# Kernel optimization log

Measured on AMD Instinct MI355X. Metric: run time of the kernel, lower is better.

The kernel has to match this reference:

```python
import jax, jax.numpy as jnp
import numpy as np

B, LQ, LK, SIZE, H = 8, 1024, 1024, 512, 8


def setup_inputs() -> dict:
    key = jax.random.key(0)
    ks = jax.random.split(key, 12)
    scale = 1.0 / np.sqrt(SIZE)
    x = jax.random.normal(ks[0], (B, LQ, SIZE), dtype=jnp.float32)
    states = jax.random.normal(ks[1], (B, LK, SIZE), dtype=jnp.float32)
    mask = jax.random.randint(ks[2], (B, LQ, LK), 0, 2, dtype=jnp.int32)
    # Per-head full-size projections, stacked over heads: [H, size, size]
    Wq = jax.random.normal(ks[3], (H, SIZE, SIZE), dtype=jnp.float32) * scale
    bq = jnp.zeros((H, SIZE), dtype=jnp.float32)
    Wk = jax.random.normal(ks[4], (H, SIZE, SIZE), dtype=jnp.float32) * scale
    bk = jnp.zeros((H, SIZE), dtype=jnp.float32)
    Wv = jax.random.normal(ks[5], (H, SIZE, SIZE), dtype=jnp.float32) * scale
    bv = jnp.zeros((H, SIZE), dtype=jnp.float32)
    # Output projection: Linear(size*H, size); torch weight shape [size, size*H]
    Wp = jax.random.normal(ks[6], (SIZE, SIZE * H), dtype=jnp.float32) * (1.0 / np.sqrt(SIZE * H))
    bp = jnp.zeros((SIZE,), dtype=jnp.float32)
    return {"x": x, "states": states, "mask": mask,
            "Wq": Wq, "bq": bq, "Wk": Wk, "bk": bk, "Wv": Wv, "bv": bv,
            "Wp": Wp, "bp": bp}


def reference(x, states, mask, Wq, bq, Wk, bk, Wv, bv, Wp, bp):
    # torch Linear: y = x @ W.T + b ; W is [out,in] so contract over last axis 'e'
    q = jnp.einsum('bqe,hde->bhqd', x, Wq) + bq[:, None, :]       # [B,H,Lq,D]
    k = jnp.einsum('bke,hde->bhkd', states, Wk) + bk[:, None, :]  # [B,H,Lk,D]
    v = jnp.einsum('bke,hde->bhkd', states, Wv) + bv[:, None, :]  # [B,H,Lk,D]
    scores = jnp.einsum('bhqd,bhkd->bhqk', q, k) / jnp.sqrt(jnp.float32(SIZE))
    scores = jnp.where(mask[:, None, :, :] == 0, jnp.float32(-jnp.inf), scores)
    attn = jax.nn.softmax(scores, axis=-1)                        # softmax over Lk
    ctx = jnp.einsum('bhqk,bhkd->bhqd', attn, v)                  # [B,H,Lq,D]
    # concat heads in order -> [B, Lq, H*D]
    ctx = ctx.transpose(0, 2, 1, 3).reshape(B, LQ, H * SIZE)
    return ctx @ Wp.T + bp
```

## Files before the change

### kernel.cpp

```cpp
#include <hip/hip_runtime.h>
#include <hip/hip_bf16.h>

typedef __bf16 bf16_t;
typedef __bf16 bf16x8 __attribute__((ext_vector_type(8)));
typedef float f32x4 __attribute__((ext_vector_type(4)));

#define B_DIM 8
#define LQ 1024
#define LK 1024
#define DD 512
#define NH 8
#define LB 2
#define NCH 4

static __device__ __forceinline__ f32x4 mfma_bf16(bf16x8 a, bf16x8 b, f32x4 c) {
  return __builtin_amdgcn_mfma_f32_16x16x32_bf16(a, b, c, 0, 0, 0);
}

static __device__ __forceinline__ void gld_lds16(const bf16_t* g, bf16_t* l) {
  __builtin_amdgcn_global_load_lds(
      (const __attribute__((address_space(1))) void*)g,
      (__attribute__((address_space(3))) void*)l, 16, 0, 0);
}

__global__ void cvt_pair(const float* __restrict__ s0, bf16_t* __restrict__ d0,
                         const float* __restrict__ s1, bf16_t* __restrict__ d1, int n) {
  const float* s = blockIdx.y ? s1 : s0;
  bf16_t* d = blockIdx.y ? d1 : d0;
  int i = (blockIdx.x * 256 + threadIdx.x) * 4;
  if (i < n) {
    const float4 f = *(const float4*)(s + i);
    bf16_t* p = d + i;
    p[0] = (bf16_t)f.x; p[1] = (bf16_t)f.y; p[2] = (bf16_t)f.z; p[3] = (bf16_t)f.w;
  }
}

__global__ void cvt_w3(const float* __restrict__ s0, const float* __restrict__ s1,
                       const float* __restrict__ s2, bf16_t* __restrict__ d0,
                       bf16_t* __restrict__ d1, bf16_t* __restrict__ d2, int n) {
  const float* s = (blockIdx.y == 0) ? s0 : (blockIdx.y == 1) ? s1 : s2;
  bf16_t* d = (blockIdx.y == 0) ? d0 : (blockIdx.y == 1) ? d1 : d2;
  int i = (blockIdx.x * 256 + threadIdx.x) * 4;
  if (i < n) {
    const float4 f = *(const float4*)(s + i);
    bf16_t* p = d + i;
    p[0] = (bf16_t)f.x; p[1] = (bf16_t)f.y; p[2] = (bf16_t)f.z; p[3] = (bf16_t)f.w;
  }
}

__global__ void cvt_f32_bf16(const float* __restrict__ s, bf16_t* __restrict__ d, int n) {
  int i = (blockIdx.x * 256 + threadIdx.x) * 4;
  if (i < n) {
    const float4 f = *(const float4*)(s + i);
    bf16_t* p = d + i;
    p[0] = (bf16_t)f.x; p[1] = (bf16_t)f.y; p[2] = (bf16_t)f.z; p[3] = (bf16_t)f.w;
  }
}

static __device__ __forceinline__ void gemm_core(
    const bf16_t* __restrict__ A, const bf16_t* __restrict__ B, int ld, int klen,
    int m0, int n0, bf16_t* As, bf16_t* Bs, f32x4 (&acc)[4][4])
{
  const int tid = threadIdx.x;
  const int wave = tid >> 6, lane = tid & 63;
  const int l15 = lane & 15, quad = lane >> 4;
  const int wm = (wave & 1) * 64, wn = (wave >> 1) * 64;

  const int r0 = tid >> 3;
  const int c8s = tid & 7;
  bf16_t* Asl = As + tid * 8;
  bf16_t* Bsl = Bs + tid * 8;

  for (int k0 = 0; k0 < klen; k0 += 64) {
    __syncthreads();
#pragma unroll
    for (int p = 0; p < 4; ++p) {
      const int r = r0 + p * 32;
      const int gc = ((c8s ^ (r & 7)) * 8) + k0;
      gld_lds16(A + (size_t)(m0 + r) * ld + gc, Asl + p * 2048);
      gld_lds16(B + (size_t)(n0 + r) * ld + gc, Bsl + p * 2048);
    }
    __syncthreads();
#pragma unroll
    for (int ks = 0; ks < 2; ++ks) {
      bf16x8 af[4], bfr[4];
#pragma unroll
      for (int i = 0; i < 4; ++i) {
        const int r = wm + i * 16 + l15;
        af[i] = *(const bf16x8*)&As[(r * 8 + ((ks * 4 + quad) ^ (r & 7))) * 8];
      }
#pragma unroll
      for (int j = 0; j < 4; ++j) {
        const int r = wn + j * 16 + l15;
        bfr[j] = *(const bf16x8*)&Bs[(r * 8 + ((ks * 4 + quad) ^ (r & 7))) * 8];
      }
#pragma unroll
      for (int i = 0; i < 4; ++i)
#pragma unroll
        for (int j = 0; j < 4; ++j)
          acc[i][j] = mfma_bf16(af[i], bfr[j], acc[i][j]);
    }
  }
}

__global__ __launch_bounds__(256, 4) void gemm_qkv(
    const bf16_t* __restrict__ xcb, const bf16_t* __restrict__ scb,
    const bf16_t* __restrict__ wq, const bf16_t* __restrict__ wk,
    const bf16_t* __restrict__ wv,
    const float* __restrict__ bq, const float* __restrict__ bk,
    const float* __restrict__ bv,
    bf16_t* __restrict__ Qc, bf16_t* __restrict__ Kc, bf16_t* __restrict__ Vtc)
{
  const int role = blockIdx.y >> 4, z = blockIdx.y & 15;
  const int bb = z >> 3, hh = z & 7;
  const int tx = blockIdx.x;

  const bf16_t* A; const bf16_t* Bm; const float* bias; bf16_t* C;
  int m0, n0, ldc, bias_row;
  if (role == 0) {
    A = xcb + (size_t)bb * LQ * DD; Bm = wq + (size_t)hh * DD * DD;
    bias = bq + hh * DD; C = Qc + (size_t)z * LQ * DD;
    m0 = (tx >> 2) * 128; n0 = (tx & 3) * 128; ldc = DD; bias_row = 0;
  } else if (role == 1) {
    A = scb + (size_t)bb * LK * DD; Bm = wk + (size_t)hh * DD * DD;
    bias = bk + hh * DD; C = Kc + (size_t)z * LK * DD;
    m0 = (tx >> 2) * 128; n0 = (tx & 3) * 128; ldc = DD; bias_row = 0;
  } else {
    A = wv + (size_t)hh * DD * DD; Bm = scb + (size_t)bb * LK * DD;
    bias = bv + hh * DD; C = Vtc + (size_t)z * DD * LK;
    m0 = (tx & 3) * 128; n0 = (tx >> 2) * 128; ldc = LK; bias_row = 1;
  }

  __shared__ __align__(16) bf16_t As[128 * 64];
  __shared__ __align__(16) bf16_t Bs[128 * 64];
  f32x4 acc[4][4];
#pragma unroll
  for (int i = 0; i < 4; ++i)
#pragma unroll
    for (int j = 0; j < 4; ++j) acc[i][j] = (f32x4){0.f, 0.f, 0.f, 0.f};

  gemm_core(A, Bm, DD, DD, m0, n0, As, Bs, acc);

  const int tid = threadIdx.x, wave = tid >> 6, lane = tid & 63;
  const int l15 = lane & 15, quad = lane >> 4;
  const int wm = (wave & 1) * 64, wn = (wave >> 1) * 64;
#pragma unroll
  for (int i = 0; i < 4; ++i)
#pragma unroll
    for (int j = 0; j < 4; ++j)
#pragma unroll
      for (int r = 0; r < 4; ++r) {
        const int row = m0 + wm + i * 16 + quad * 4 + r;
        const int col = n0 + wn + j * 16 + l15;
        const float v = acc[i][j][r] + (bias_row ? bias[row] : bias[col]);
        C[(size_t)row * ldc + col] = (bf16_t)v;
      }
}

__global__ __launch_bounds__(256, 4) void gemm_qk(
    const bf16_t* __restrict__ Q, const bf16_t* __restrict__ K,
    const int* __restrict__ mask, bf16_t* __restrict__ S, float* __restrict__ rs)
{
  const int z = blockIdx.z, bb = z >> 3, nt = blockIdx.y;
  const bf16_t* Az = Q + (size_t)z * LQ * DD;
  const bf16_t* Bz = K + (size_t)z * LK * DD;
  bf16_t* Sz = S + (size_t)z * LQ * LK;
  const int* mz = mask + (size_t)bb * LQ * LK;

  const int m0 = blockIdx.x * 128, n0 = nt * 128;
  __shared__ __align__(16) bf16_t As[128 * 64];
  __shared__ __align__(16) bf16_t Bs[128 * 64];
  f32x4 acc[4][4];
#pragma unroll
  for (int i = 0; i < 4; ++i)
#pragma unroll
    for (int j = 0; j < 4; ++j) acc[i][j] = (f32x4){0.f, 0.f, 0.f, 0.f};

  gemm_core(Az, Bz, DD, DD, m0, n0, As, Bs, acc);

  const int tid = threadIdx.x, wave = tid >> 6, lane = tid & 63;
  const int l15 = lane & 15, quad = lane >> 4;
  const int wm = (wave & 1) * 64, wn = (wave >> 1) * 64;
  float* rsz = rs + (((size_t)z * 8 + nt) * 2 + (wave >> 1)) * LQ;
  const float scale = 0.04419417382415922f;

#pragma unroll
  for (int i = 0; i < 4; ++i)
#pragma unroll
    for (int r = 0; r < 4; ++r) {
      const int row = m0 + wm + i * 16 + quad * 4 + r;
      float rsum = 0.f;
#pragma unroll
      for (int j = 0; j < 4; ++j) {
        const int col = n0 + wn + j * 16 + l15;
        const int mv = mz[(size_t)row * LK + col];
        const float p = mv ? __expf(acc[i][j][r] * scale) : 0.f;
        rsum += p;
        Sz[(size_t)row * LK + col] = (bf16_t)p;
      }
      rsum += __shfl_xor(rsum, 1);
      rsum += __shfl_xor(rsum, 2);
      rsum += __shfl_xor(rsum, 4);
      rsum += __shfl_xor(rsum, 8);
      if (l15 == 0) rsz[row] = rsum;
    }
}

__global__ __launch_bounds__(256, 4) void gemm_pv(
    const bf16_t* __restrict__ S, const bf16_t* __restrict__ Vt,
    const float* __restrict__ rs, bf16_t* __restrict__ ctx)
{
  const int z = blockIdx.z, bb = z >> 3, hh = z & 7;
  const bf16_t* Az = S + (size_t)z * LQ * LK;
  const bf16_t* Bz = Vt + (size_t)z * DD * LK;
  bf16_t* Cz = ctx + (size_t)bb * LQ * (NH * DD) + (size_t)hh * DD;

  const int m0 = blockIdx.x * 128, n0 = blockIdx.y * 128;
  __shared__ __align__(16) bf16_t As[128 * 64];
  __shared__ __align__(16) bf16_t Bs[128 * 64];
  __shared__ float invs[128];

  const int tid = threadIdx.x;
  if (tid < 128) {
    const float* p = rs + (size_t)z * 16 * LQ + (m0 + tid);
    float tot = 0.f;
#pragma unroll
    for (int s = 0; s < 16; ++s) tot += p[s * LQ];
    invs[tid] = 1.f / tot;
  }

  f32x4 acc[4][4];
#pragma unroll
  for (int i = 0; i < 4; ++i)
#pragma unroll
    for (int j = 0; j < 4; ++j) acc[i][j] = (f32x4){0.f, 0.f, 0.f, 0.f};

  gemm_core(Az, Bz, LK, LK, m0, n0, As, Bs, acc);

  const int wave = tid >> 6, lane = tid & 63;
  const int l15 = lane & 15, quad = lane >> 4;
  const int wm = (wave & 1) * 64, wn = (wave >> 1) * 64;

#pragma unroll
  for (int i = 0; i < 4; ++i)
#pragma unroll
    for (int r = 0; r < 4; ++r) {
      const int lrow = wm + i * 16 + quad * 4 + r;
      const float iv = invs[lrow];
#pragma unroll
      for (int j = 0; j < 4; ++j) {
        const int col = n0 + wn + j * 16 + l15;
        Cz[(size_t)(m0 + lrow) * (NH * DD) + col] = (bf16_t)(acc[i][j][r] * iv);
      }
    }
}

__global__ __launch_bounds__(256, 4) void gemm_outk(
    const bf16_t* __restrict__ ctx, const bf16_t* __restrict__ wp,
    float* __restrict__ partial)
{
  const int ks = blockIdx.z;
  const bf16_t* A = ctx + ks * 1024;
  const bf16_t* B = wp + ks * 1024;
  float* P = partial + (size_t)ks * B_DIM * LQ * DD;

  const int m0 = blockIdx.x * 128, n0 = blockIdx.y * 128;
  __shared__ __align__(16) bf16_t As[128 * 64];
  __shared__ __align__(16) bf16_t Bs[128 * 64];
  f32x4 acc[4][4];
#pragma unroll
  for (int i = 0; i < 4; ++i)
#pragma unroll
    for (int j = 0; j < 4; ++j) acc[i][j] = (f32x4){0.f, 0.f, 0.f, 0.f};

  gemm_core(A, B, NH * DD, 1024, m0, n0, As, Bs, acc);

  const int tid = threadIdx.x, wave = tid >> 6, lane = tid & 63;
  const int l15 = lane & 15, quad = lane >> 4;
  const int wm = (wave & 1) * 64, wn = (wave >> 1) * 64;
#pragma unroll
  for (int i = 0; i < 4; ++i)
#pragma unroll
    for (int j = 0; j < 4; ++j)
#pragma unroll
      for (int r = 0; r < 4; ++r) {
        const int row = m0 + wm + i * 16 + quad * 4 + r;
        const int col = n0 + wn + j * 16 + l15;
        P[(size_t)row * DD + col] = acc[i][j][r];
      }
}

__global__ void reduce_out(const float* __restrict__ p, const float* __restrict__ bp,
                           float* __restrict__ out) {
  const int N = B_DIM * LQ * DD;
  int i = (blockIdx.x * 256 + threadIdx.x) * 4;
  float4 a = *(const float4*)(p + i);
  float4 b = *(const float4*)(p + N + i);
  float4 c = *(const float4*)(p + 2 * N + i);
  float4 d = *(const float4*)(p + 3 * N + i);
  const float4 bb4 = *(const float4*)(bp + (i & 511));
  float4 r;
  r.x = a.x + b.x + c.x + d.x + bb4.x;
  r.y = a.y + b.y + c.y + d.y + bb4.y;
  r.z = a.z + b.z + c.z + d.z + bb4.z;
  r.w = a.w + b.w + c.w + d.w + bb4.w;
  *(float4*)(out + i) = r;
}

extern "C" void kernel_launch(void* const* d_in, const int* in_sizes, int n_in,
                              void* d_out, int out_size, void* d_ws, size_t ws_size,
                              hipStream_t stream) {
  const float* x      = (const float*)d_in[0];
  const float* states = (const float*)d_in[1];
  const int*   mask   = (const int*)d_in[2];
  const float* Wq     = (const float*)d_in[3];
  const float* bq     = (const float*)d_in[4];
  const float* Wk     = (const float*)d_in[5];
  const float* bk     = (const float*)d_in[6];
  const float* Wv     = (const float*)d_in[7];
  const float* bv     = (const float*)d_in[8];
  const float* Wp     = (const float*)d_in[9];
  const float* bp     = (const float*)d_in[10];
  float* out = (float*)d_out;

  char* ws = (char*)d_ws;
  bf16_t* ctxb = (bf16_t*)(ws + 0);
  bf16_t* wqb  = (bf16_t*)(ws + 67108864);
  bf16_t* wkb  = (bf16_t*)(ws + 71303168);
  bf16_t* wvb  = (bf16_t*)(ws + 75497472);
  bf16_t* Qc   = (bf16_t*)(ws + 79691776);
  bf16_t* Kc   = (bf16_t*)(ws + 96468992);
  bf16_t* Vtc  = (bf16_t*)(ws + 113246208);
  bf16_t* Sb   = (bf16_t*)(ws + 130023424);
  bf16_t* xcb  = (bf16_t*)(ws + 163577856);
  bf16_t* scb  = (bf16_t*)(ws + 165675008);
  bf16_t* wpb  = Qc;
  float*  pbuf = (float*)(ws + 96468992);
  float*  rsum = out;

  const int n_w = NH * DD * DD;
  const int n_xc = LB * LQ * DD;

  cvt_w3<<<dim3(n_w / 1024, 3), 256, 0, stream>>>(Wq, Wk, Wv, wqb, wkb, wvb, n_w);

  for (int c = 0; c < NCH; ++c) {
    const float* xc = x + (size_t)c * LB * LQ * DD;
    const float* sc = states + (size_t)c * LB * LK * DD;
    const int* mc = mask + (size_t)c * LB * LQ * LK;
    bf16_t* ctxc = ctxb + (size_t)c * LB * LQ * (NH * DD);

    cvt_pair<<<dim3(n_xc / 1024, 2), 256, 0, stream>>>(xc, xcb, sc, scb, n_xc);

    gemm_qkv<<<dim3(32, 3 * LB * NH), 256, 0, stream>>>(
        xcb, scb, wqb, wkb, wvb, bq, bk, bv, Qc, Kc, Vtc);

    gemm_qk<<<dim3(8, 8, LB * NH), 256, 0, stream>>>(Qc, Kc, mc, Sb, rsum);
    gemm_pv<<<dim3(8, 4, LB * NH), 256, 0, stream>>>(Sb, Vtc, rsum, ctxc);
  }

  cvt_f32_bf16<<<n_w / 1024, 256, 0, stream>>>(Wp, wpb, n_w);
  gemm_outk<<<dim3(64, 4, 4), 256, 0, stream>>>(ctxb, wpb, pbuf);
  reduce_out<<<(B_DIM * LQ * DD) / 1024, 256, 0, stream>>>(pbuf, bp, out);
}
```

Measured before the change: 604.2 us.

## Use 256x256 double-buffered GEMM core with interleaved prefetch for QKV, QK, out-proj

Adds a new GEMM core that uses 512-thread blocks computing 256x256 output tiles. K-tiles are double-buffered in LDS through direct global-to-LDS loads, and LDS fragment reads and next-tile prefetches are interleaved with four MFMA quadrants. Barriers and s_setprio separate the phases. The QKV projection, QK score and output-projection kernels switch to this core with retuned grids, and the row-sum partial layout in the QK epilogue is remapped to keep 16 partials per row. The aim is more operand reuse per LDS byte and load latency hidden behind MFMA work. In exchange it needs 128KB of LDS per block (one block per CU), uses many accumulator registers, and the QKV grid of 384 blocks may leave a partial wave.

Result: slower. 659.2 us (+9.1%).

```diff
diff --git a/kernel.cpp b/kernel.cpp
--- a/kernel.cpp
+++ b/kernel.cpp
@@ -103,7 +103,111 @@
   }
 }
 
-__global__ __launch_bounds__(256, 4) void gemm_qkv(
+#define SBAR() __builtin_amdgcn_s_barrier()
+#define SETPRIO(x) __builtin_amdgcn_s_setprio(x)
+#define LGKM0() do { asm volatile("s_waitcnt lgkmcnt(0)" ::: "memory"); \
+                     __builtin_amdgcn_sched_barrier(0); } while (0)
+#define VMC(n) asm volatile("s_waitcnt vmcnt(" #n ")" ::: "memory")
+
+static __device__ __forceinline__ void gemm256_core(
+    const bf16_t* __restrict__ A, const bf16_t* __restrict__ Bm,
+    const int ld, const int nkt, const int m0, const int n0,
+    bf16_t* __restrict__ As, bf16_t* __restrict__ Bs, f32x4 (&acc)[8][4])
+{
+  const int tid = threadIdx.x;
+  const int wave = tid >> 6, lane = tid & 63;
+  const int l15 = lane & 15, quad = lane >> 4;
+  const int wm = ((wave >> 2) & 1) << 4;
+  const int wn = (wave & 3) << 4;
+
+  const int s1 = tid + 512;
+  const int r0 = tid >> 3, r1 = s1 >> 3;
+  const int g0 = ((tid & 7) ^ (r0 & 7)) << 3;
+  const int g1 = ((s1 & 7) ^ (r1 & 7)) << 3;
+  const bf16_t* pa0 = A + (size_t)(m0 + r0) * ld + g0;
+  const bf16_t* pa1 = A + (size_t)(m0 + r1) * ld + g1;
+  const bf16_t* pb0 = Bm + (size_t)(n0 + r0) * ld + g0;
+  const bf16_t* pb1 = Bm + (size_t)(n0 + r1) * ld + g1;
+  const size_t hgl = (size_t)128 * ld;
+  bf16_t* la = As + tid * 8;
+  bf16_t* lb = Bs + tid * 8;
+
+#define STG_A(kt, h) do { const int _o = (((kt) & 1) << 14) + ((h) << 13); \
+    const size_t _g = (size_t)(h) * hgl + ((kt) << 6); \
+    gld_lds16(pa0 + _g, la + _o); gld_lds16(pa1 + _g, la + _o + 4096); } while (0)
+#define STG_B(kt, h) do { const int _o = (((kt) & 1) << 14) + ((h) << 13); \
+    const size_t _g = (size_t)(h) * hgl + ((kt) << 6); \
+    gld_lds16(pb0 + _g, lb + _o); gld_lds16(pb1 + _g, lb + _o + 4096); } while (0)
+
+  bf16x8 af[2][4][2];
+  bf16x8 bfrag[2][2];
+
+#define RD_A(mh) do { _Pragma("unroll") for (int a = 0; a < 4; ++a) { \
+    const int rl = wm + a * 32 + l15; \
+    const int rb = sb + ((mh) << 13) + rl * 64; \
+    _Pragma("unroll") for (int ks = 0; ks < 2; ++ks) \
+      af[mh][a][ks] = *(const bf16x8*)&As[rb + (((ks * 4 + quad) ^ (rl & 7)) << 3)]; \
+  } } while (0)
+#define RD_B(nh) do { _Pragma("unroll") for (int b = 0; b < 2; ++b) { \
+    const int rl = wn + b * 64 + l15; \
+    const int rb = sb + ((nh) << 13) + rl * 64; \
+    _Pragma("unroll") for (int ks = 0; ks < 2; ++ks) \
+      bfrag[b][ks] = *(const bf16x8*)&Bs[rb + (((ks * 4 + quad) ^ (rl & 7)) << 3)]; \
+  } } while (0)
+#define MMA(mh, nh) do { _Pragma("unroll") for (int ks = 0; ks < 2; ++ks) \
+    _Pragma("unroll") for (int a = 0; a < 4; ++a) \
+    _Pragma("unroll") for (int b = 0; b < 2; ++b) \
+      acc[(mh) * 4 + a][(nh) * 2 + b] = \
+          mfma_bf16(af[mh][a][ks], bfrag[b][ks], acc[(mh) * 4 + a][(nh) * 2 + b]); \
+  } while (0)
+
+  STG_A(0, 0); STG_A(0, 1); STG_B(0, 0); STG_B(0, 1);
+  if (nkt > 1) {
+    STG_A(1, 0); STG_A(1, 1); STG_B(1, 0); STG_B(1, 1);
+    VMC(8);
+  } else {
+    VMC(0);
+  }
+  SBAR();
+
+#pragma unroll 2
+  for (int kt = 0; kt < nkt; ++kt) {
+    const int sb = (kt & 1) << 14;
+    const int kt2 = kt + 2;
+    const bool pf = kt2 < nkt;
+    RD_A(0); RD_B(0);
+    SBAR(); LGKM0();
+    SETPRIO(1); MMA(0, 0); SETPRIO(0);
+    SBAR();
+    RD_A(1);
+    if (pf) { STG_A(kt2, 0); STG_B(kt2, 0); }
+    SBAR(); LGKM0();
+    SETPRIO(1); MMA(1, 0); SETPRIO(0);
+    SBAR();
+    RD_B(1);
+    if (pf) STG_A(kt2, 1);
+    SBAR(); LGKM0();
+    SETPRIO(1); MMA(0, 1); SETPRIO(0);
+    SBAR();
+    if (pf) STG_B(kt2, 1);
+    SBAR(); LGKM0();
+    SETPRIO(1); MMA(1, 1); SETPRIO(0);
+    if (kt < nkt - 1) {
+      if (pf) { VMC(8); } else { VMC(0); }
+      SBAR();
+    }
+  }
+#undef STG_A
+#undef STG_B
+#undef RD_A
+#undef RD_B
+#undef MMA
+}
+
+#define ROW256(i, r) (m0 + (((i) >> 2) << 7) + wm + ((i) & 3) * 32 + quad * 4 + (r))
+#define COL256(j)    (n0 + (((j) >> 1) << 7) + wn + ((j) & 1) * 64 + l15)
+
+__global__ __launch_bounds__(512, 2) void gemm_qkv(
     const bf16_t* __restrict__ xcb, const bf16_t* __restrict__ scb,
     const bf16_t* __restrict__ wq, const bf16_t* __restrict__ wk,
     const bf16_t* __restrict__ wv,
@@ -120,79 +224,79 @@
   if (role == 0) {
     A = xcb + (size_t)bb * LQ * DD; Bm = wq + (size_t)hh * DD * DD;
     bias = bq + hh * DD; C = Qc + (size_t)z * LQ * DD;
-    m0 = (tx >> 2) * 128; n0 = (tx & 3) * 128; ldc = DD; bias_row = 0;
+    m0 = (tx >> 1) * 256; n0 = (tx & 1) * 256; ldc = DD; bias_row = 0;
   } else if (role == 1) {
     A = scb + (size_t)bb * LK * DD; Bm = wk + (size_t)hh * DD * DD;
     bias = bk + hh * DD; C = Kc + (size_t)z * LK * DD;
-    m0 = (tx >> 2) * 128; n0 = (tx & 3) * 128; ldc = DD; bias_row = 0;
+    m0 = (tx >> 1) * 256; n0 = (tx & 1) * 256; ldc = DD; bias_row = 0;
   } else {
     A = wv + (size_t)hh * DD * DD; Bm = scb + (size_t)bb * LK * DD;
     bias = bv + hh * DD; C = Vtc + (size_t)z * DD * LK;
-    m0 = (tx & 3) * 128; n0 = (tx >> 2) * 128; ldc = LK; bias_row = 1;
-  }
-
-  __shared__ __align__(16) bf16_t As[128 * 64];
-  __shared__ __align__(16) bf16_t Bs[128 * 64];
-  f32x4 acc[4][4];
-#pragma unroll
-  for (int i = 0; i < 4; ++i)
+    m0 = (tx & 1) * 256; n0 = (tx >> 1) * 256; ldc = LK; bias_row = 1;
+  }
+
+  __shared__ __align__(16) bf16_t As[32768];
+  __shared__ __align__(16) bf16_t Bs[32768];
+  f32x4 acc[8][4];
+#pragma unroll
+  for (int i = 0; i < 8; ++i)
 #pragma unroll
     for (int j = 0; j < 4; ++j) acc[i][j] = (f32x4){0.f, 0.f, 0.f, 0.f};
 
-  gemm_core(A, Bm, DD, DD, m0, n0, As, Bs, acc);
+  gemm256_core(A, Bm, DD, DD / 64, m0, n0, As, Bs, acc);
 
   const int tid = threadIdx.x, wave = tid >> 6, lane = tid & 63;
   const int l15 = lane & 15, quad = lane >> 4;
-  const int wm = (wave & 1) * 64, wn = (wave >> 1) * 64;
-#pragma unroll
-  for (int i = 0; i < 4; ++i)
+  const int wm = ((wave >> 2) & 1) << 4, wn = (wave & 3) << 4;
+#pragma unroll
+  for (int i = 0; i < 8; ++i)
 #pragma unroll
     for (int j = 0; j < 4; ++j)
 #pragma unroll
       for (int r = 0; r < 4; ++r) {
-        const int row = m0 + wm + i * 16 + quad * 4 + r;
-        const int col = n0 + wn + j * 16 + l15;
+        const int row = ROW256(i, r);
+        const int col = COL256(j);
         const float v = acc[i][j][r] + (bias_row ? bias[row] : bias[col]);
         C[(size_t)row * ldc + col] = (bf16_t)v;
       }
 }
 
-__global__ __launch_bounds__(256, 4) void gemm_qk(
+__global__ __launch_bounds__(512, 2) void gemm_qk(
     const bf16_t* __restrict__ Q, const bf16_t* __restrict__ K,
     const int* __restrict__ mask, bf16_t* __restrict__ S, float* __restrict__ rs)
 {
-  const int z = blockIdx.z, bb = z >> 3, nt = blockIdx.y;
+  const int z = blockIdx.z, bb = z >> 3, by = blockIdx.y;
   const bf16_t* Az = Q + (size_t)z * LQ * DD;
   const bf16_t* Bz = K + (size_t)z * LK * DD;
   bf16_t* Sz = S + (size_t)z * LQ * LK;
   const int* mz = mask + (size_t)bb * LQ * LK;
 
-  const int m0 = blockIdx.x * 128, n0 = nt * 128;
-  __shared__ __align__(16) bf16_t As[128 * 64];
-  __shared__ __align__(16) bf16_t Bs[128 * 64];
-  f32x4 acc[4][4];
-#pragma unroll
-  for (int i = 0; i < 4; ++i)
+  const int m0 = blockIdx.x * 256, n0 = by * 256;
+  __shared__ __align__(16) bf16_t As[32768];
+  __shared__ __align__(16) bf16_t Bs[32768];
+  f32x4 acc[8][4];
+#pragma unroll
+  for (int i = 0; i < 8; ++i)
 #pragma unroll
     for (int j = 0; j < 4; ++j) acc[i][j] = (f32x4){0.f, 0.f, 0.f, 0.f};
 
-  gemm_core(Az, Bz, DD, DD, m0, n0, As, Bs, acc);
+  gemm256_core(Az, Bz, DD, DD / 64, m0, n0, As, Bs, acc);
 
   const int tid = threadIdx.x, wave = tid >> 6, lane = tid & 63;
   const int l15 = lane & 15, quad = lane >> 4;
-  const int wm = (wave & 1) * 64, wn = (wave >> 1) * 64;
-  float* rsz = rs + (((size_t)z * 8 + nt) * 2 + (wave >> 1)) * LQ;
+  const int wm = ((wave >> 2) & 1) << 4, wn = (wave & 3) << 4;
+  float* rsz = rs + (((size_t)z * 4 + by) * 4 + (wave & 3)) * LQ;
   const float scale = 0.04419417382415922f;
 
 #pragma unroll
-  for (int i = 0; i < 4; ++i)
+  for (int i = 0; i < 8; ++i)
 #pragma unroll
     for (int r = 0; r < 4; ++r) {
-      const int row = m0 + wm + i * 16 + quad * 4 + r;
+      const int row = ROW256(i, r);
       float rsum = 0.f;
 #pragma unroll
       for (int j = 0; j < 4; ++j) {
-        const int col = n0 + wn + j * 16 + l15;
+        const int col = COL256(j);
         const int mv = mz[(size_t)row * LK + col];
         const float p = mv ? __expf(acc[i][j][r] * scale) : 0.f;
         rsum += p;
@@ -255,7 +359,7 @@
     }
 }
 
-__global__ __launch_bounds__(256, 4) void gemm_outk(
+__global__ __launch_bounds__(512, 2) void gemm_outk(
     const bf16_t* __restrict__ ctx, const bf16_t* __restrict__ wp,
     float* __restrict__ partial)
 {
@@ -264,28 +368,28 @@
   const bf16_t* B = wp + ks * 1024;
   float* P = partial + (size_t)ks * B_DIM * LQ * DD;
 
-  const int m0 = blockIdx.x * 128, n0 = blockIdx.y * 128;
-  __shared__ __align__(16) bf16_t As[128 * 64];
-  __shared__ __align__(16) bf16_t Bs[128 * 64];
-  f32x4 acc[4][4];
-#pragma unroll
-  for (int i = 0; i < 4; ++i)
+  const int m0 = blockIdx.x * 256, n0 = blockIdx.y * 256;
+  __shared__ __align__(16) bf16_t As[32768];
+  __shared__ __align__(16) bf16_t Bs[32768];
+  f32x4 acc[8][4];
+#pragma unroll
+  for (int i = 0; i < 8; ++i)
 #pragma unroll
     for (int j = 0; j < 4; ++j) acc[i][j] = (f32x4){0.f, 0.f, 0.f, 0.f};
 
-  gemm_core(A, B, NH * DD, 1024, m0, n0, As, Bs, acc);
+  gemm256_core(A, B, NH * DD, 1024 / 64, m0, n0, As, Bs, acc);
 
   const int tid = threadIdx.x, wave = tid >> 6, lane = tid & 63;
   const int l15 = lane & 15, quad = lane >> 4;
-  const int wm = (wave & 1) * 64, wn = (wave >> 1) * 64;
-#pragma unroll
-  for (int i = 0; i < 4; ++i)
+  const int wm = ((wave >> 2) & 1) << 4, wn = (wave & 3) << 4;
+#pragma unroll
+  for (int i = 0; i < 8; ++i)
 #pragma unroll
     for (int j = 0; j < 4; ++j)
 #pragma unroll
       for (int r = 0; r < 4; ++r) {
-        const int row = m0 + wm + i * 16 + quad * 4 + r;
-        const int col = n0 + wn + j * 16 + l15;
+        const int row = ROW256(i, r);
+        const int col = COL256(j);
         P[(size_t)row * DD + col] = acc[i][j][r];
       }
 }
@@ -351,14 +455,14 @@
 
     cvt_pair<<<dim3(n_xc / 1024, 2), 256, 0, stream>>>(xc, xcb, sc, scb, n_xc);
 
-    gemm_qkv<<<dim3(32, 3 * LB * NH), 256, 0, stream>>>(
+    gemm_qkv<<<dim3(8, 3 * LB * NH), 512, 0, stream>>>(
         xcb, scb, wqb, wkb, wvb, bq, bk, bv, Qc, Kc, Vtc);
 
-    gemm_qk<<<dim3(8, 8, LB * NH), 256, 0, stream>>>(Qc, Kc, mc, Sb, rsum);
+    gemm_qk<<<dim3(4, 4, LB * NH), 512, 0, stream>>>(Qc, Kc, mc, Sb, rsum);
     gemm_pv<<<dim3(8, 4, LB * NH), 256, 0, stream>>>(Sb, Vtc, rsum, ctxc);
   }
 
   cvt_f32_bf16<<<n_w / 1024, 256, 0, stream>>>(Wp, wpb, n_w);
-  gemm_outk<<<dim3(64, 4, 4), 256, 0, stream>>>(ctxb, wpb, pbuf);
+  gemm_outk<<<dim3(32, 2, 4), 512, 0, stream>>>(ctxb, wpb, pbuf);
   reduce_out<<<(B_DIM * LQ * DD) / 1024, 256, 0, stream>>>(pbuf, bp, out);
 }
```
